# Optimization experiments

Measured on AMD Instinct MI355X. Metric: run time of the kernel, lower is better.

## Reference

```python
import jax, jax.numpy as jnp
import numpy as np

# Tsit5 (Tsitouras 2011) explicit RK tableau coefficients (5th-order solution weights)
A21 = 0.161
A31, A32 = -0.008480655492356989, 0.335480655492357
A41, A42, A43 = 2.8971530571054935, -6.359448489975075, 4.3622954328695815
A51, A52, A53, A54 = 5.325864828439257, -11.748883564062828, 7.4955393428898365, -0.09249506636175525
A61, A62, A63, A64, A65 = 5.86145544294642, -12.92096931784711, 8.159367898576159, -0.071584973281401, -0.028269050394068383
B1, B2, B3, B4, B5, B6 = 0.09646076681806523, 0.01, 0.4798896504144996, 1.379008574103742, -3.290069515436081, 2.324710524099774

BATCH, D, H, T = 4096, 64, 256, 128


def net_apply(y, W1, b1, W2, b2):
    # y: [B, D] -> dy/dt: [B, D]  (MLP vector field, autonomous)
    return jnp.tanh(y @ W1 + b1) @ W2 + b2


def tsit5_step(f, y, h):
    # One explicit Tsit5 step of size h on state y: [B, D]
    k1 = f(y)
    k2 = f(y + h * (A21 * k1))
    k3 = f(y + h * (A31 * k1 + A32 * k2))
    k4 = f(y + h * (A41 * k1 + A42 * k2 + A43 * k3))
    k5 = f(y + h * (A51 * k1 + A52 * k2 + A53 * k3 + A54 * k4))
    k6 = f(y + h * (A61 * k1 + A62 * k2 + A63 * k3 + A64 * k4 + A65 * k5))
    return y + h * (B1 * k1 + B2 * k2 + B3 * k3 + B4 * k4 + B5 * k5 + B6 * k6)


def setup_inputs() -> dict:
    key = jax.random.key(0)
    k0, k1, k2 = jax.random.split(key, 3)
    y0 = jax.random.normal(k0, (BATCH, D), dtype=jnp.float32)
    ts = jnp.arange(T, dtype=jnp.float32) * 0.05  # save times
    W1 = jax.random.normal(k1, (D, H), dtype=jnp.float32) / np.sqrt(D)
    b1 = jnp.zeros((H,), dtype=jnp.float32)
    W2 = jax.random.normal(k2, (H, D), dtype=jnp.float32) / np.sqrt(H)
    b2 = jnp.zeros((D,), dtype=jnp.float32)
    return {"y0": y0, "ts": ts, "W1": W1, "b1": b1, "W2": W2, "b2": b2, "n_sub": 8}


def reference(y0, ts, W1, b1, W2, b2, n_sub):
    # Integrate dy/dt = net(y) with fixed-step Tsit5 (n_sub substeps per save interval),
    # returning the trajectory at save points ts: [B, T, D].
    f = lambda y: net_apply(y, W1, b1, W2, b2)

    def interval(y, dt):
        h = dt / n_sub
        def sub(yc, _):
            return tsit5_step(f, yc, h), None
        y, _ = jax.lax.scan(sub, y, None, length=n_sub)
        return y, y

    dts = jnp.diff(ts)                      # [T-1]
    _, ys = jax.lax.scan(interval, y0, dts)  # [T-1, B, D]
    traj = jnp.concatenate([y0[None], ys], axis=0)  # [T, B, D]
    return jnp.transpose(traj, (1, 0, 2))   # [B, T, D]
```

## Files before the change

### kernel.cpp

```cpp
#include <hip/hip_runtime.h>
#include <hip/hip_bf16.h>

typedef __bf16 bf16x8 __attribute__((ext_vector_type(8)));
typedef float f32x4 __attribute__((ext_vector_type(4)));
typedef unsigned int u32;
typedef u32 u32x4 __attribute__((ext_vector_type(4)));

#define MFMA_B16(a,b,c) __builtin_amdgcn_mfma_f32_16x16x32_bf16((a),(b),(c),0,0,0)

#define A21f 0.161f
#define A31f (-0.008480655492356989f)
#define A32f 0.335480655492357f
#define A41f 2.8971530571054935f
#define A42f (-6.359448489975075f)
#define A43f 4.3622954328695815f
#define A51f 5.325864828439257f
#define A52f (-11.748883564062828f)
#define A53f 7.4955393428898365f
#define A54f (-0.09249506636175525f)
#define A61f 5.86145544294642f
#define A62f (-12.92096931784711f)
#define A63f 8.159367898576159f
#define A64f (-0.071584973281401f)
#define A65f (-0.028269050394068383f)
#define B1f 0.09646076681806523f
#define B2f 0.01f
#define B3f 0.4798896504144996f
#define B4f 1.379008574103742f
#define B5f (-3.290069515436081f)
#define B6f 2.324710524099774f

constexpr int T_SAVE = 128;
constexpr int DIM = 64;
constexpr int HID = 256;

__device__ __forceinline__ float fast_exp2(float x){
#if __has_builtin(__builtin_amdgcn_exp2f)
  return __builtin_amdgcn_exp2f(x);
#else
  return exp2f(x);
#endif
}
__device__ __forceinline__ float fast_rcp(float x){
#if __has_builtin(__builtin_amdgcn_rcpf)
  return __builtin_amdgcn_rcpf(x);
#else
  return 1.0f / x;
#endif
}
__device__ __forceinline__ float tanh_fast(float x){
  float t = fast_exp2(x * 2.8853900817779268f);
  return 1.0f - 2.0f * fast_rcp(t + 1.0f);
}
__device__ __forceinline__ f32x4 splat4(float x){ return f32x4{x,x,x,x}; }

__device__ __forceinline__ u32 pack_hl(float x){
  u32 xu = __float_as_uint(x);
  float lo = x - __uint_as_float(xu & 0xFFFF0000u);
  __bf16 lb = (__bf16)lo;
  unsigned short ls; __builtin_memcpy(&ls, &lb, 2);
  return ((u32)ls << 16) | (xu >> 16);
}

__device__ __forceinline__ void unpack_hl(const u32* p, bf16x8& ah, bf16x8& al){
  union { u32 d[4]; bf16x8 v; } H, L;
#pragma unroll
  for (int j = 0; j < 4; ++j) {
    H.d[j] = __builtin_amdgcn_perm(p[2*j+1], p[2*j], 0x05040100u);
    L.d[j] = __builtin_amdgcn_perm(p[2*j+1], p[2*j], 0x07060302u);
  }
  ah = H.v; al = L.v;
}

__global__ __launch_bounds__(512, 2)
void node_tsit5_kernel(const float* __restrict__ y0, const float* __restrict__ ts,
                       const float* __restrict__ W1g, const float* __restrict__ b1g,
                       const float* __restrict__ W2g, const float* __restrict__ b2g,
                       const int* __restrict__ nsub_p, float* __restrict__ out)
{
  const int tid = (int)threadIdx.x;
  const int w   = tid >> 6;
  const int l   = tid & 63;
  const int c   = l & 15;
  const int g   = l >> 4;
  const bool state = (w < 4);
  const int tile = state ? w : (w - 4);
  const int kh   = state ? 0 : 1;
  const int rowbase = (int)blockIdx.x * 16;

  __shared__ __align__(16) u32 Yp[1024];
  __shared__ __align__(16) u32 Hp[4096];
  __shared__ __align__(16) f32x4 Pex[256];
  __shared__ float ts_s[T_SAVE];

  if (tid < T_SAVE) ts_s[tid] = ts[tid];

  const int nsub = nsub_p[0];

  bf16x8 w1h[2][2], w1l[2][2];
#pragma unroll
  for (int nt = 0; nt < 2; ++nt) {
    const int col = (2*w + nt)*16 + c;
#pragma unroll
    for (int s = 0; s < 2; ++s)
#pragma unroll
      for (int j = 0; j < 8; ++j) {
        float v = W1g[(s*32 + g*8 + j)*HID + col];
        __bf16 hi = (__bf16)v;
        w1h[nt][s][j] = hi;
        w1l[nt][s][j] = (__bf16)(v - (float)hi);
      }
  }
  bf16x8 w2h[4], w2l[4];
#pragma unroll
  for (int i = 0; i < 4; ++i) {
    const int ks = 4*kh + i;
#pragma unroll
    for (int j = 0; j < 8; ++j) {
      float v = W2g[(ks*32 + g*8 + j)*DIM + (tile*16 + c)];
      __bf16 hi = (__bf16)v;
      w2h[i][j] = hi;
      w2l[i][j] = (__bf16)(v - (float)hi);
    }
  }
  float b1v[2];
#pragma unroll
  for (int nt = 0; nt < 2; ++nt) b1v[nt] = b1g[(2*w + nt)*16 + c];
  const float b2v = b2g[tile*16 + c];

  const int rdDw = (l ^ ((l >> 2) & 3)) * 8;

  int hoffDw[2][4];
#pragma unroll
  for (int nt = 0; nt < 2; ++nt)
#pragma unroll
    for (int r = 0; r < 4; ++r)
      hoffDw[nt][r] = w*512 + (nt*2 + (c>>3))*128 + 32*g + 8*(r ^ g) + (c & 7);
  int yoffDw[4];
#pragma unroll
  for (int s = 0; s < 4; ++s)
    yoffDw[s] = (w>>1)*512 + ((w&1)*2 + (c>>3))*128 + 32*g + 8*(s ^ g) + (c & 7);

  const int d_ = tile*16 + c;
  f32x4 y4 = {0.f,0.f,0.f,0.f};
  if (state) {
#pragma unroll
    for (int s = 0; s < 4; ++s) {
      int row = rowbase + 4*g + s;
      y4[s] = y0[row*DIM + d_];
      out[(size_t)row*(T_SAVE*DIM) + d_] = y4[s];
    }
  }
  __syncthreads();

  f32x4 ysv = y4;

  auto feval = [&]() -> f32x4 {
    if (state) {
#pragma unroll
      for (int s = 0; s < 4; ++s) Yp[yoffDw[s]] = pack_hl(ysv[s]);
    }
    __syncthreads();
    u32 py[8], pz[8];
    *(u32x4*)&py[0] = *(const u32x4*)&Yp[rdDw];
    *(u32x4*)&py[4] = *(const u32x4*)&Yp[rdDw + 4];
    *(u32x4*)&pz[0] = *(const u32x4*)&Yp[512 + rdDw];
    *(u32x4*)&pz[4] = *(const u32x4*)&Yp[512 + rdDw + 4];
    bf16x8 ah0, al0, ah1, al1;
    unpack_hl(py, ah0, al0);
    unpack_hl(pz, ah1, al1);
    f32x4 t0a={0.f,0.f,0.f,0.f}, t0b={0.f,0.f,0.f,0.f};
    f32x4 t1a={0.f,0.f,0.f,0.f}, t1b={0.f,0.f,0.f,0.f};
    t0a = MFMA_B16(ah0, w1h[0][0], t0a);  t0b = MFMA_B16(ah1, w1h[0][1], t0b);
    t1a = MFMA_B16(ah0, w1h[1][0], t1a);  t1b = MFMA_B16(ah1, w1h[1][1], t1b);
    t0a = MFMA_B16(ah0, w1l[0][0], t0a);  t0b = MFMA_B16(ah1, w1l[0][1], t0b);
    t1a = MFMA_B16(ah0, w1l[1][0], t1a);  t1b = MFMA_B16(ah1, w1l[1][1], t1b);
    t0a = MFMA_B16(al0, w1h[0][0], t0a);  t0b = MFMA_B16(al1, w1h[0][1], t0b);
    t1a = MFMA_B16(al0, w1h[1][0], t1a);  t1b = MFMA_B16(al1, w1h[1][1], t1b);
    f32x4 ht0 = t0a + t0b, ht1 = t1a + t1b;
#pragma unroll
    for (int r = 0; r < 4; ++r)
      Hp[hoffDw[0][r]] = pack_hl(tanh_fast(ht0[r] + b1v[0]));
#pragma unroll
    for (int r = 0; r < 4; ++r)
      Hp[hoffDw[1][r]] = pack_hl(tanh_fast(ht1[r] + b1v[1]));
    __syncthreads();
    u32 ph[4][8];
#pragma unroll
    for (int i = 0; i < 4; ++i) {
      const int ks = 4*kh + i;
      *(u32x4*)&ph[i][0] = *(const u32x4*)&Hp[ks*512 + rdDw];
      *(u32x4*)&ph[i][4] = *(const u32x4*)&Hp[ks*512 + rdDw + 4];
    }
    f32x4 aA={0.f,0.f,0.f,0.f}, aB={0.f,0.f,0.f,0.f}, aC={0.f,0.f,0.f,0.f};
#pragma unroll
    for (int i = 0; i < 4; ++i) {
      bf16x8 ah, al;
      unpack_hl(ph[i], ah, al);
      aA = MFMA_B16(ah, w2h[i], aA);
      aB = MFMA_B16(ah, w2l[i], aB);
      aC = MFMA_B16(al, w2h[i], aC);
    }
    f32x4 part = (aA + aB) + aC;
    if (!state) Pex[tile*64 + l] = part;
    __syncthreads();
    f32x4 kout = {0.f,0.f,0.f,0.f};
    if (state) {
      f32x4 q = Pex[tile*64 + l];
      kout = (part + q) + splat4(b2v);
    }
    return kout;
  };

  for (int iv = 0; iv < T_SAVE-1; ++iv) {
    const float h = (ts_s[iv+1] - ts_s[iv]) / (float)nsub;
    const f32x4 h4 = splat4(h);
    for (int sub = 0; sub < nsub; ++sub) {
      f32x4 k1 = feval();
      if (state) ysv = y4 + h4 * (splat4(A21f) * k1);
      f32x4 k2 = feval();
      if (state) {
        f32x4 t = splat4(A31f)*k1 + splat4(A32f)*k2;
        ysv = y4 + h4 * t;
      }
      f32x4 k3 = feval();
      if (state) {
        f32x4 t = splat4(A41f)*k1 + splat4(A42f)*k2 + splat4(A43f)*k3;
        ysv = y4 + h4 * t;
      }
      f32x4 k4 = feval();
      if (state) {
        f32x4 t = splat4(A51f)*k1 + splat4(A52f)*k2 + splat4(A53f)*k3
                + splat4(A54f)*k4;
        ysv = y4 + h4 * t;
      }
      f32x4 k5 = feval();
      if (state) {
        f32x4 t = splat4(A61f)*k1 + splat4(A62f)*k2 + splat4(A63f)*k3
                + splat4(A64f)*k4 + splat4(A65f)*k5;
        ysv = y4 + h4 * t;
      }
      f32x4 k6 = feval();
      if (state) {
        f32x4 t = splat4(B1f)*k1 + splat4(B2f)*k2 + splat4(B3f)*k3
                + splat4(B4f)*k4 + splat4(B5f)*k5 + splat4(B6f)*k6;
        y4 = y4 + h4 * t;
        ysv = y4;
      }
    }
    if (state) {
#pragma unroll
      for (int s = 0; s < 4; ++s) {
        int row = rowbase + 4*g + s;
        out[(size_t)row*(T_SAVE*DIM) + (size_t)(iv+1)*DIM + d_] = y4[s];
      }
    }
  }
}

extern "C" void kernel_launch(void* const* d_in, const int* in_sizes, int n_in,
                              void* d_out, int out_size, void* d_ws, size_t ws_size,
                              hipStream_t stream) {
  const float* y0 = (const float*)d_in[0];
  const float* ts = (const float*)d_in[1];
  const float* W1 = (const float*)d_in[2];
  const float* b1 = (const float*)d_in[3];
  const float* W2 = (const float*)d_in[4];
  const float* b2 = (const float*)d_in[5];
  const int* nsub = (const int*)d_in[6];
  float* out = (float*)d_out;

  const int Bnum = in_sizes[0] / DIM;
  const int nblocks = Bnum / 16;
  node_tsit5_kernel<<<nblocks, 512, 0, stream>>>(y0, ts, W1, b1, W2, b2, nsub, out);
}
```

Before: 7.348 ms.

## Split waves into layer-1 and layer-2 specialists, drop partial-sum exchange barrier

Reassigns work so the four non-state waves compute the full hidden layer and the four state waves compute the full output layer over all K, removing the Pex partial-sum exchange and one block barrier per function evaluation. LDS layouts for Y and H are re-swizzled with a new bank mapping. The trade-off is that each wave group does twice the MFMA work while the other group idles, lengthening the per-eval critical path unless other resident blocks fill the gaps.

```diff
diff --git a/kernel.cpp b/kernel.cpp
--- a/kernel.cpp
+++ b/kernel.cpp
@@ -61,8 +61,7 @@
   unsigned short ls; __builtin_memcpy(&ls, &lb, 2);
   return ((u32)ls << 16) | (xu >> 16);
 }
-
-__device__ __forceinline__ void unpack_hl(const u32* p, bf16x8& ah, bf16x8& al){
+__device__ __forceinline__ void unpack2(const u32* p, bf16x8& ah, bf16x8& al){
   union { u32 d[4]; bf16x8 v; } H, L;
 #pragma unroll
   for (int j = 0; j < 4; ++j) {
@@ -70,6 +69,10 @@
     L.d[j] = __builtin_amdgcn_perm(p[2*j+1], p[2*j], 0x07060302u);
   }
   ah = H.v; al = L.v;
+}
+
+__device__ __forceinline__ int bphys(int row, int kq){
+  return kq*16 + (row & 8) + ((row & 7) ^ (kq & 7));
 }
 
 __global__ __launch_bounds__(512, 2)
@@ -84,64 +87,69 @@
   const int c   = l & 15;
   const int g   = l >> 4;
   const bool state = (w < 4);
-  const int tile = state ? w : (w - 4);
-  const int kh   = state ? 0 : 1;
+  const int v   = state ? w : (w - 4);
   const int rowbase = (int)blockIdx.x * 16;
 
   __shared__ __align__(16) u32 Yp[1024];
   __shared__ __align__(16) u32 Hp[4096];
-  __shared__ __align__(16) f32x4 Pex[256];
   __shared__ float ts_s[T_SAVE];
 
   if (tid < T_SAVE) ts_s[tid] = ts[tid];
 
   const int nsub = nsub_p[0];
 
-  bf16x8 w1h[2][2], w1l[2][2];
-#pragma unroll
-  for (int nt = 0; nt < 2; ++nt) {
-    const int col = (2*w + nt)*16 + c;
-#pragma unroll
-    for (int s = 0; s < 2; ++s)
+  bf16x8 wf[16];
+  float bias[4];
+  if (state) {
+#pragma unroll
+    for (int ks = 0; ks < 8; ++ks)
 #pragma unroll
       for (int j = 0; j < 8; ++j) {
-        float v = W1g[(s*32 + g*8 + j)*HID + col];
-        __bf16 hi = (__bf16)v;
-        w1h[nt][s][j] = hi;
-        w1l[nt][s][j] = (__bf16)(v - (float)hi);
-      }
-  }
-  bf16x8 w2h[4], w2l[4];
-#pragma unroll
-  for (int i = 0; i < 4; ++i) {
-    const int ks = 4*kh + i;
-#pragma unroll
-    for (int j = 0; j < 8; ++j) {
-      float v = W2g[(ks*32 + g*8 + j)*DIM + (tile*16 + c)];
-      __bf16 hi = (__bf16)v;
-      w2h[i][j] = hi;
-      w2l[i][j] = (__bf16)(v - (float)hi);
-    }
-  }
-  float b1v[2];
-#pragma unroll
-  for (int nt = 0; nt < 2; ++nt) b1v[nt] = b1g[(2*w + nt)*16 + c];
-  const float b2v = b2g[tile*16 + c];
-
-  const int rdDw = (l ^ ((l >> 2) & 3)) * 8;
-
-  int hoffDw[2][4];
-#pragma unroll
-  for (int nt = 0; nt < 2; ++nt)
-#pragma unroll
-    for (int r = 0; r < 4; ++r)
-      hoffDw[nt][r] = w*512 + (nt*2 + (c>>3))*128 + 32*g + 8*(r ^ g) + (c & 7);
-  int yoffDw[4];
-#pragma unroll
-  for (int s = 0; s < 4; ++s)
-    yoffDw[s] = (w>>1)*512 + ((w&1)*2 + (c>>3))*128 + 32*g + 8*(s ^ g) + (c & 7);
-
-  const int d_ = tile*16 + c;
+        float val = W2g[(ks*32 + g*8 + j)*DIM + (v*16 + c)];
+        __bf16 hi = (__bf16)val;
+        wf[ks*2    ][j] = hi;
+        wf[ks*2 + 1][j] = (__bf16)(val - (float)hi);
+      }
+    bias[0] = b2g[v*16 + c];
+    bias[1] = bias[2] = bias[3] = 0.f;
+  } else {
+#pragma unroll
+    for (int t = 0; t < 4; ++t) {
+      const int col = (v*4 + t)*16 + c;
+#pragma unroll
+      for (int sl = 0; sl < 2; ++sl)
+#pragma unroll
+        for (int j = 0; j < 8; ++j) {
+          float val = W1g[(sl*32 + g*8 + j)*HID + col];
+          __bf16 hi = (__bf16)val;
+          wf[t*4 + sl*2    ][j] = hi;
+          wf[t*4 + sl*2 + 1][j] = (__bf16)(val - (float)hi);
+        }
+      bias[t] = b1g[col];
+    }
+  }
+
+  const int rdw0 = bphys(c, 2*g    ) * 4;
+  const int rdw1 = bphys(c, 2*g + 1) * 4;
+  int yw[4];
+#pragma unroll
+  for (int s = 0; s < 4; ++s) {
+    const int kq = (v & 1)*4 + (c >> 2);
+    yw[s] = ((v >> 1)*512) + bphys(4*g + s, kq)*4 + (c & 3);
+  }
+  int hw[4][4];
+  if (!state) {
+#pragma unroll
+    for (int t = 0; t < 4; ++t) {
+      const int T = v*4 + t;
+      const int kq = (T & 1)*4 + (c >> 2);
+#pragma unroll
+      for (int r = 0; r < 4; ++r)
+        hw[t][r] = ((T >> 1)*512) + bphys(4*g + r, kq)*4 + (c & 3);
+    }
+  }
+
+  const int d_ = v*16 + c;
   f32x4 y4 = {0.f,0.f,0.f,0.f};
   if (state) {
 #pragma unroll
@@ -158,58 +166,54 @@
   auto feval = [&]() -> f32x4 {
     if (state) {
 #pragma unroll
-      for (int s = 0; s < 4; ++s) Yp[yoffDw[s]] = pack_hl(ysv[s]);
+      for (int s = 0; s < 4; ++s) Yp[yw[s]] = pack_hl(ysv[s]);
     }
     __syncthreads();
-    u32 py[8], pz[8];
-    *(u32x4*)&py[0] = *(const u32x4*)&Yp[rdDw];
-    *(u32x4*)&py[4] = *(const u32x4*)&Yp[rdDw + 4];
-    *(u32x4*)&pz[0] = *(const u32x4*)&Yp[512 + rdDw];
-    *(u32x4*)&pz[4] = *(const u32x4*)&Yp[512 + rdDw + 4];
-    bf16x8 ah0, al0, ah1, al1;
-    unpack_hl(py, ah0, al0);
-    unpack_hl(pz, ah1, al1);
-    f32x4 t0a={0.f,0.f,0.f,0.f}, t0b={0.f,0.f,0.f,0.f};
-    f32x4 t1a={0.f,0.f,0.f,0.f}, t1b={0.f,0.f,0.f,0.f};
-    t0a = MFMA_B16(ah0, w1h[0][0], t0a);  t0b = MFMA_B16(ah1, w1h[0][1], t0b);
-    t1a = MFMA_B16(ah0, w1h[1][0], t1a);  t1b = MFMA_B16(ah1, w1h[1][1], t1b);
-    t0a = MFMA_B16(ah0, w1l[0][0], t0a);  t0b = MFMA_B16(ah1, w1l[0][1], t0b);
-    t1a = MFMA_B16(ah0, w1l[1][0], t1a);  t1b = MFMA_B16(ah1, w1l[1][1], t1b);
-    t0a = MFMA_B16(al0, w1h[0][0], t0a);  t0b = MFMA_B16(al1, w1h[0][1], t0b);
-    t1a = MFMA_B16(al0, w1h[1][0], t1a);  t1b = MFMA_B16(al1, w1h[1][1], t1b);
-    f32x4 ht0 = t0a + t0b, ht1 = t1a + t1b;
-#pragma unroll
-    for (int r = 0; r < 4; ++r)
-      Hp[hoffDw[0][r]] = pack_hl(tanh_fast(ht0[r] + b1v[0]));
-#pragma unroll
-    for (int r = 0; r < 4; ++r)
-      Hp[hoffDw[1][r]] = pack_hl(tanh_fast(ht1[r] + b1v[1]));
+    if (!state) {
+      u32 py[2][8];
+      *(u32x4*)&py[0][0] = *(const u32x4*)&Yp[rdw0];
+      *(u32x4*)&py[0][4] = *(const u32x4*)&Yp[rdw1];
+      *(u32x4*)&py[1][0] = *(const u32x4*)&Yp[512 + rdw0];
+      *(u32x4*)&py[1][4] = *(const u32x4*)&Yp[512 + rdw1];
+      bf16x8 ah[2], al[2];
+      unpack2(py[0], ah[0], al[0]);
+      unpack2(py[1], ah[1], al[1]);
+#pragma unroll
+      for (int t = 0; t < 4; ++t) {
+        f32x4 a0 = {0.f,0.f,0.f,0.f}, a1 = {0.f,0.f,0.f,0.f};
+        a0 = MFMA_B16(ah[0], wf[t*4 + 0], a0);
+        a1 = MFMA_B16(ah[1], wf[t*4 + 2], a1);
+        a0 = MFMA_B16(ah[0], wf[t*4 + 1], a0);
+        a1 = MFMA_B16(ah[1], wf[t*4 + 3], a1);
+        a0 = MFMA_B16(al[0], wf[t*4 + 0], a0);
+        a1 = MFMA_B16(al[1], wf[t*4 + 2], a1);
+        f32x4 ht = a0 + a1;
+#pragma unroll
+        for (int r = 0; r < 4; ++r)
+          Hp[hw[t][r]] = pack_hl(tanh_fast(ht[r] + bias[t]));
+      }
+    }
     __syncthreads();
-    u32 ph[4][8];
-#pragma unroll
-    for (int i = 0; i < 4; ++i) {
-      const int ks = 4*kh + i;
-      *(u32x4*)&ph[i][0] = *(const u32x4*)&Hp[ks*512 + rdDw];
-      *(u32x4*)&ph[i][4] = *(const u32x4*)&Hp[ks*512 + rdDw + 4];
-    }
-    f32x4 aA={0.f,0.f,0.f,0.f}, aB={0.f,0.f,0.f,0.f}, aC={0.f,0.f,0.f,0.f};
-#pragma unroll
-    for (int i = 0; i < 4; ++i) {
-      bf16x8 ah, al;
-      unpack_hl(ph[i], ah, al);
-      aA = MFMA_B16(ah, w2h[i], aA);
-      aB = MFMA_B16(ah, w2l[i], aB);
-      aC = MFMA_B16(al, w2h[i], aC);
-    }
-    f32x4 part = (aA + aB) + aC;
-    if (!state) Pex[tile*64 + l] = part;
-    __syncthreads();
-    f32x4 kout = {0.f,0.f,0.f,0.f};
+    f32x4 ret = {0.f,0.f,0.f,0.f};
     if (state) {
-      f32x4 q = Pex[tile*64 + l];
-      kout = (part + q) + splat4(b2v);
-    }
-    return kout;
+      u32 ph[8][8];
+#pragma unroll
+      for (int ks = 0; ks < 8; ++ks) {
+        *(u32x4*)&ph[ks][0] = *(const u32x4*)&Hp[ks*512 + rdw0];
+        *(u32x4*)&ph[ks][4] = *(const u32x4*)&Hp[ks*512 + rdw1];
+      }
+      f32x4 aA = {0.f,0.f,0.f,0.f}, aB = {0.f,0.f,0.f,0.f}, aC = {0.f,0.f,0.f,0.f};
+#pragma unroll
+      for (int ks = 0; ks < 8; ++ks) {
+        bf16x8 ah, al;
+        unpack2(ph[ks], ah, al);
+        aA = MFMA_B16(ah, wf[ks*2    ], aA);
+        aB = MFMA_B16(ah, wf[ks*2 + 1], aB);
+        aC = MFMA_B16(al, wf[ks*2    ], aC);
+      }
+      ret = (aA + aB) + aC + splat4(bias[0]);
+    }
+    return ret;
   };
 
   for (int iv = 0; iv < T_SAVE-1; ++iv) {
```

After: 7.646 ms. 4.0% more time.
